# Optimization experiments

Hardware: AMD Instinct MI355X
Metric: run time of the kernel (lower is better)

The kernel has to match this reference:

```python
import jax, jax.numpy as jnp
import numpy as np

B, T, NHANDS, DKP = 8, 1024, 2, 128
DM, H, DH, DFF, V, M, L = 1024, 16, 64, 4096, 2000, 256, 2
KEPS = 1e-4  # performer feature-map epsilon


def _orth_proj(key, m, d):
    # Gaussian orthogonal random features (FAVOR+), rows rescaled to chi norms
    n_blocks = int(np.ceil(m / d))
    blocks = []
    for i in range(n_blocks):
        q, _ = jnp.linalg.qr(jax.random.normal(jax.random.fold_in(key, i), (d, d)))
        blocks.append(q.T)
    mat = jnp.concatenate(blocks, 0)[:m]
    mult = jnp.linalg.norm(jax.random.normal(jax.random.fold_in(key, 10 ** 6), (m, d)), axis=1)
    return (mat * mult[:, None]).astype(jnp.float32)


def setup_inputs() -> dict:
    key = jax.random.key(0)
    ks = iter(jax.random.split(key, 64))
    w = lambda shape, s=0.02: (jax.random.normal(next(ks), shape) * s).astype(jnp.float32)
    z = lambda *shape: jnp.zeros(shape, jnp.float32)
    o = lambda *shape: jnp.ones(shape, jnp.float32)
    return {
        'x': jax.random.normal(next(ks), (B, T, NHANDS, DKP), dtype=jnp.float32),
        'Win': w((NHANDS * DKP, DM)), 'b_in': z(DM),
        'pe': jax.random.normal(next(ks), (5000, DM), dtype=jnp.float32),
        'ln1_g': o(L, DM), 'ln1_b': z(L, DM),
        'Wq': w((L, DM, DM)), 'bq': z(L, DM),
        'Wk': w((L, DM, DM)), 'bk': z(L, DM),
        'Wv': w((L, DM, DM)), 'bv': z(L, DM),
        'Wo': w((L, DM, DM)), 'bo': z(L, DM),
        'ln2_g': o(L, DM), 'ln2_b': z(L, DM),
        'W1': w((L, DM, DFF)), 'b1': z(L, DFF),
        'W2': w((L, DFF, DM)), 'b2': z(L, DM),
        'Wc': w((DM, V)), 'bc': z(V),
        'Wconv': w((64, DM, 3)), 'bconv': z(64),
        'Waux': w((64, V + 1)), 'baux': z(V + 1),
        'proj': _orth_proj(next(ks), M, DH),
    }


def _ln(x, g, b):
    mu = jnp.mean(x, -1, keepdims=True)
    var = jnp.mean((x - mu) ** 2, -1, keepdims=True)
    return (x - mu) / jnp.sqrt(var + 1e-5) * g + b


def _feats(data, proj, is_query):
    # FAVOR+ softmax kernel features, data: (B,H,T,DH) -> (B,H,T,M)
    dn = DH ** -0.25
    ratio = M ** -0.5
    dd = jnp.einsum('bhnd,md->bhnm', data, proj) * dn
    diag = jnp.sum(data ** 2, -1, keepdims=True) * 0.5 * dn * dn
    if is_query:
        stab = jnp.max(dd, -1, keepdims=True)
    else:
        stab = jnp.max(dd, (-1, -2), keepdims=True)
    return ratio * (jnp.exp(dd - diag - jax.lax.stop_gradient(stab)) + KEPS)


def reference(x, Win, b_in, pe, ln1_g, ln1_b, Wq, bq, Wk, bk, Wv, bv, Wo, bo,
              ln2_g, ln2_b, W1, b1, W2, b2, Wc, bc, Wconv, bconv, Waux, baux, proj):
    h = x.reshape(B, T, NHANDS * DKP) @ Win + b_in
    h = h + pe[:T][None]

    def layer(h, i):
        y = _ln(h, ln1_g[i], ln1_b[i])
        q = (y @ Wq[i] + bq[i]).reshape(B, T, H, DH).transpose(0, 2, 1, 3)
        k = (y @ Wk[i] + bk[i]).reshape(B, T, H, DH).transpose(0, 2, 1, 3)
        v = (y @ Wv[i] + bv[i]).reshape(B, T, H, DH).transpose(0, 2, 1, 3)
        qp = _feats(q, proj, True)   # (B,H,T,M)
        kp = _feats(k, proj, False)
        dinv = 1.0 / jnp.einsum('bhnm,bhm->bhn', qp, kp.sum(2))
        ctx = jnp.einsum('bhnm,bhnd->bhmd', kp, v)          # (B,H,M,DH)
        o = jnp.einsum('bhnm,bhmd->bhnd', qp, ctx) * dinv[..., None]
        o = o.transpose(0, 2, 1, 3).reshape(B, T, DM) @ Wo[i] + bo[i]
        h = h + o
        y = _ln(h, ln2_g[i], ln2_b[i])
        ff = jax.nn.gelu(y @ W1[i] + b1[i], approximate=False) @ W2[i] + b2[i]
        return h + ff

    h = layer(h, 0)
    xa = h.transpose(0, 2, 1)  # (B, DM, T)
    xa = jax.lax.conv_general_dilated(xa, Wconv, (1,), 'SAME',
                                      dimension_numbers=('NCH', 'OIH', 'NCH'))
    xa = xa + bconv[None, :, None]
    aux = xa.transpose(0, 2, 1) @ Waux + baux  # (B, T, V+1)
    h = layer(h, 1)
    gloss = h @ Wc + bc  # (B, T, V)
    return (gloss, aux)
```

## Files before the change

### kernel.cpp

```cpp
#include <hip/hip_runtime.h>
#include <hip/hip_bf16.h>

typedef __attribute__((ext_vector_type(4))) float f32x4;
typedef __attribute__((ext_vector_type(8))) unsigned short u16x8;
typedef __attribute__((ext_vector_type(4))) unsigned short u16x4;
typedef __bf16 bf16x8 __attribute__((ext_vector_type(8)));

#define DEVFN static __device__ __forceinline__

constexpr int CB = 8, CT = 1024, CDM = 1024, CH = 16, CDH = 64, CDFF = 4096, CV = 2000, CM = 256;
constexpr int CNT = CB * CT;
constexpr int CQKV = 3072;
constexpr float CDN = 0.35355339059327373f;
constexpr float CRATIO = 0.0625f;
constexpr float CKEPS = 1e-4f;

DEVFN unsigned short f2bu(float x) {
  __hip_bfloat16 h = __float2bfloat16(x);
  return __builtin_bit_cast(unsigned short, h);
}
DEVFN float b2f(unsigned short u) {
  __hip_bfloat16 h = __builtin_bit_cast(__hip_bfloat16, u);
  return __bfloat162float(h);
}
DEVFN float wredsum(float s) {
#pragma unroll
  for (int ofs = 32; ofs; ofs >>= 1) s += __shfl_xor(s, ofs, 64);
  return s;
}
DEVFN float wredmax(float s) {
#pragma unroll
  for (int ofs = 32; ofs; ofs >>= 1) s = fmaxf(s, __shfl_xor(s, ofs, 64));
  return s;
}
DEVFN void gl_lds16(const void* g, void* l) {
  __builtin_amdgcn_global_load_lds(
      (const __attribute__((address_space(1))) unsigned int*)g,
      (__attribute__((address_space(3))) unsigned int*)l, 16, 0, 0);
}
DEVFN f32x4 mfma16(u16x8 a, u16x8 b, f32x4 c) {
  return __builtin_amdgcn_mfma_f32_16x16x32_bf16(
      __builtin_bit_cast(bf16x8, a), __builtin_bit_cast(bf16x8, b), c, 0, 0, 0);
}
DEVFN u16x8 lds_rd128(unsigned addr) {
  u16x8 r;
  asm volatile("ds_read_b128 %0, %1" : "=v"(r) : "v"(addr));
  return r;
}
DEVFN unsigned lds_addr(const void* p) {
  return (unsigned)(unsigned long)(const __attribute__((address_space(3))) char*)p;
}

#define EPI_BIAS 1
#define EPI_ACCUM 2
#define EPI_GELU 4
#define EPI_OUTBF 8
#define EPI_PE 32
#define EPI_DUP 64

template <int EPI>
__global__ __launch_bounds__(512, 4) void gemm128_k(
    const unsigned short* __restrict__ A, const unsigned short* __restrict__ Bt,
    const float* __restrict__ bias, void* __restrict__ C, void* __restrict__ aux,
    int Mr, int Nr, int Kr, int lda, int ldb, int ldc) {
  __shared__ unsigned short smA[2][128 * 64];
  __shared__ unsigned short smB[2][128 * 64];

  int tid = threadIdx.x, wv = tid >> 6, ll = tid & 63;
  int wm = wv >> 2, wn = wv & 3;
  int m0 = blockIdx.x * 128, n0 = blockIdx.y * 128;
  int fr = ll & 15, f16 = ll >> 4, fk = f16 * 8;

  const char* Ab = (const char*)A;
  const char* Bb = (const char*)Bt;

  unsigned int offA[2], offB[2];
#pragma unroll
  for (int ro = 0; ro < 2; ro++) {
    int L = (ro * 512 + tid) * 16;
    int P = L ^ (((L >> 9) & 1) << 5);
    int kh = P >> 13, rem = P & 8191;
    int r = rem >> 6, cb = rem & 63;
    long rowA = min(m0 + r, Mr - 1);
    offA[ro] = (unsigned)((rowA * lda + kh * 32) * 2 + cb);
    long rowB = min(n0 + r, Nr - 1);
    offB[ro] = (unsigned)((rowB * ldb + kh * 32) * 2 + cb);
  }
  unsigned aAb = lds_addr(&smA[0][0]), aBb = lds_addr(&smB[0][0]);
  unsigned offArd[4], offBrd[2];
#pragma unroll
  for (int i = 0; i < 4; i++) {
    int r = wm * 64 + i * 16 + fr;
    offArd[i] = aAb + (unsigned)(r * 64 + 2 * (fk ^ (((r >> 3) & 1) << 4)));
  }
#pragma unroll
  for (int j = 0; j < 2; j++) {
    int r = wn * 32 + j * 16 + fr;
    offBrd[j] = aBb + (unsigned)(r * 64 + 2 * (fk ^ (((r >> 3) & 1) << 4)));
  }

  f32x4 acc[4][2] = {};
  int NT = Kr / 64;

#define STGALL(PB, KBN)                                                      \
  {                                                                          \
    _Pragma("unroll") for (int ro = 0; ro < 2; ro++)                         \
        gl_lds16(Ab + offA[ro] + (KBN), &smA[PB][(ro * 512 + wv * 64) * 8]); \
    _Pragma("unroll") for (int ro = 0; ro < 2; ro++)                         \
        gl_lds16(Bb + offB[ro] + (KBN), &smB[PB][(ro * 512 + wv * 64) * 8]); \
  }
#define TILE(PB, KBN)                                                        \
  {                                                                          \
    __builtin_amdgcn_s_barrier();                                            \
    __builtin_amdgcn_sched_barrier(0);                                       \
    STGALL((PB) ^ 1, KBN);                                                   \
    asm volatile("s_waitcnt vmcnt(4)" ::: "memory");                         \
    __builtin_amdgcn_sched_barrier(0);                                       \
    __builtin_amdgcn_s_barrier();                                            \
    __builtin_amdgcn_sched_barrier(0);                                       \
    u16x8 a0[4], b0[2], a1[4], b1[2];                                        \
    _Pragma("unroll") for (int i = 0; i < 4; i++)                            \
        a0[i] = lds_rd128(offArd[i] + (PB)*16384);                           \
    _Pragma("unroll") for (int j = 0; j < 2; j++)                            \
        b0[j] = lds_rd128(offBrd[j] + (PB)*16384);                           \
    _Pragma("unroll") for (int i = 0; i < 4; i++)                            \
        a1[i] = lds_rd128(offArd[i] + (PB)*16384 + 8192);                    \
    _Pragma("unroll") for (int j = 0; j < 2; j++)                            \
        b1[j] = lds_rd128(offBrd[j] + (PB)*16384 + 8192);                    \
    asm volatile("s_waitcnt lgkmcnt(6)" ::: "memory");                       \
    __builtin_amdgcn_sched_barrier(0);                                       \
    __builtin_amdgcn_s_setprio(1);                                           \
    _Pragma("unroll") for (int i = 0; i < 4; i++) {                          \
      acc[i][0] = mfma16(a0[i], b0[0], acc[i][0]);                           \
      acc[i][1] = mfma16(a0[i], b0[1], acc[i][1]);                           \
    }                                                                        \
    __builtin_amdgcn_s_setprio(0);                                           \
    asm volatile("s_waitcnt lgkmcnt(0)" ::: "memory");                       \
    __builtin_amdgcn_sched_barrier(0);                                       \
    __builtin_amdgcn_s_setprio(1);                                           \
    _Pragma("unroll") for (int i = 0; i < 4; i++) {                          \
      acc[i][0] = mfma16(a1[i], b1[0], acc[i][0]);                           \
      acc[i][1] = mfma16(a1[i], b1[1], acc[i][1]);                           \
    }                                                                        \
    __builtin_amdgcn_s_setprio(0);                                           \
  }

  STGALL(0, 0);
  for (int t = 0; t < NT; t += 2) {
    long kb1 = (long)(t + 1) * 128;
    long kb2 = (long)min(t + 2, NT - 1) * 128;
    TILE(0, kb1);
    TILE(1, kb2);
  }
  asm volatile("s_waitcnt vmcnt(0)" ::: "memory");
  __builtin_amdgcn_sched_barrier(0);
#undef TILE
#undef STGALL

#pragma unroll
  for (int i = 0; i < 4; i++) {
#pragma unroll
    for (int j = 0; j < 2; j++) {
#pragma unroll
      for (int e = 0; e < 4; e++) {
        int gr = m0 + wm * 64 + i * 16 + f16 * 4 + e;
        int gc = n0 + wn * 32 + j * 16 + fr;
        if (gr < Mr && gc < Nr) {
          float v = acc[i][j][e];
          if (EPI & EPI_BIAS) v += bias[gc];
          if (EPI & EPI_GELU) v = 0.5f * v * (1.0f + erff(v * 0.70710678118f));
          if (EPI & EPI_PE) v += ((const float*)aux)[((long)(gr & 1023) << 10) + gc];
          long idx = (long)gr * ldc + gc;
          if (EPI & EPI_ACCUM) v += ((float*)C)[idx];
          if (EPI & EPI_OUTBF) ((unsigned short*)C)[idx] = f2bu(v);
          else ((float*)C)[idx] = v;
          if (EPI & EPI_DUP) ((unsigned short*)aux)[idx] = f2bu(v);
        }
      }
    }
  }
}

template <int EPI, int MB, int NB>
__global__ __launch_bounds__(256) void gemm_k(
    const unsigned short* __restrict__ Aall, const unsigned short* __restrict__ Btall,
    const float* __restrict__ bias, void* __restrict__ Call,
    int Mr, int Nr, int Kr, int lda, int ldb, int ldc, int bdiv,
    long As1, long As2, long Bs1, long Bs2, long Cs1, long Cs2) {
  __shared__ unsigned short smA[MB * 32];
  __shared__ unsigned short smB[NB * 32];
  constexpr int WRN = (MB == 128 && NB == 128) ? 2 : (MB == 128 ? 4 : 1);
  constexpr int WCN = 4 / WRN;
  constexpr int MT = MB / WRN, NTW = NB / WCN;
  constexpr int AF = MT / 16, BF = NTW / 16;
  int bz = blockIdx.z;
  const unsigned short* A = Aall + (long)(bz / bdiv) * As1 + (long)(bz % bdiv) * As2;
  const unsigned short* Bt = Btall + (long)(bz / bdiv) * Bs1 + (long)(bz % bdiv) * Bs2;
  long coff = (long)(bz / bdiv) * Cs1 + (long)(bz % bdiv) * Cs2;

  int tid = threadIdx.x, wv = tid >> 6, ll = tid & 63;
  int m0 = blockIdx.x * MB, n0 = blockIdx.y * NB;
  int sr = tid >> 2, sc = (tid & 3) * 8;
  long ar0 = min(m0 + sr, Mr - 1);
  long ar1 = (MB == 128) ? min(m0 + sr + 64, (long)Mr - 1) : 0;
  long br0 = min(n0 + sr, Nr - 1);
  long br1 = (NB == 128) ? min(n0 + sr + 64, (long)Nr - 1) : 0;
  unsigned short* lA0 = &smA[(wv * 16) * 32];
  unsigned short* lA1 = &smA[(64 + wv * 16) * 32];
  unsigned short* lB0 = &smB[(wv * 16) * 32];
  unsigned short* lB1 = &smB[(64 + wv * 16) * 32];

  f32x4 acc[AF][BF] = {};
  int wr = (WRN == 1) ? 0 : ((WRN == 2) ? (wv >> 1) * MT : wv * MT);
  int wc = (WCN == 1) ? 0 : ((WCN == 2) ? (wv & 1) * NTW : wv * NTW);
  int fr = ll & 15, fk = (ll >> 4) * 8;

  for (int k0 = 0; k0 < Kr; k0 += 32) {
    __syncthreads();
    gl_lds16(A + ar0 * lda + k0 + sc, lA0);
    if (MB == 128) gl_lds16(A + ar1 * lda + k0 + sc, lA1);
    gl_lds16(Bt + br0 * ldb + k0 + sc, lB0);
    if (NB == 128) gl_lds16(Bt + br1 * ldb + k0 + sc, lB1);
    __syncthreads();
    u16x8 af[AF], bfr[BF];
#pragma unroll
    for (int i = 0; i < AF; i++) af[i] = *(const u16x8*)&smA[(wr + i * 16 + fr) * 32 + fk];
#pragma unroll
    for (int j = 0; j < BF; j++) bfr[j] = *(const u16x8*)&smB[(wc + j * 16 + fr) * 32 + fk];
#pragma unroll
    for (int i = 0; i < AF; i++)
#pragma unroll
      for (int j = 0; j < BF; j++) acc[i][j] = mfma16(af[i], bfr[j], acc[i][j]);
  }

#pragma unroll
  for (int i = 0; i < AF; i++) {
#pragma unroll
    for (int j = 0; j < BF; j++) {
#pragma unroll
      for (int e = 0; e < 4; e++) {
        int gr = m0 + wr + i * 16 + (ll >> 4) * 4 + e;
        int gc = n0 + wc + j * 16 + (ll & 15);
        if (gr < Mr && gc < Nr) {
          float v = acc[i][j][e];
          if (EPI & EPI_BIAS) v += bias[gc];
          long idx = coff + (long)gr * ldc + gc;
          if (EPI & EPI_OUTBF) ((unsigned short*)Call)[idx] = f2bu(v);
          else ((float*)Call)[idx] = v;
        }
      }
    }
  }
}

DEVFN void feat_dd(const unsigned short* __restrict__ src, const unsigned short* __restrict__ projc,
                   unsigned short* ldsq, unsigned short* ldsp, int b, int t0, int hh,
                   f32x4 acc[16]) {
  int tid = threadIdx.x, wv = tid >> 6, ll = tid & 63;
#pragma unroll
  for (int p = 0; p < 2; p++) {
    int r = p * 64 + (tid >> 3), c8 = (tid & 7) * 8;
    *(u16x8*)&ldsq[r * 72 + c8] =
        *(const u16x8*)&src[((long)b * CT + t0 + r) * CQKV + hh * CDH + c8];
  }
#pragma unroll
  for (int p = 0; p < 4; p++) {
    int r = p * 64 + (tid >> 3), c8 = (tid & 7) * 8;
    *(u16x8*)&ldsp[r * 72 + c8] = *(const u16x8*)&projc[r * 64 + c8];
  }
  __syncthreads();
  int fr = ll & 15, fk = (ll >> 4) * 8;
#pragma unroll
  for (int ks = 0; ks < 2; ks++) {
    u16x8 af = *(const u16x8*)&ldsq[(wv * 16 + fr) * 72 + ks * 32 + fk];
#pragma unroll
    for (int j = 0; j < 16; j++) {
      u16x8 bf = *(const u16x8*)&ldsp[(j * 16 + fr) * 72 + ks * 32 + fk];
      acc[j] = mfma16(af, bf, acc[j]);
    }
  }
}

__global__ __launch_bounds__(512, 4) void kstab_f(const unsigned short* __restrict__ kb,
                                                  const unsigned short* __restrict__ projc,
                                                  float* __restrict__ part) {
  extern __shared__ char dynsm[];
  unsigned short* ldsq = (unsigned short*)dynsm;
  unsigned short* ldsp = (unsigned short*)(dynsm + 18432);
  __shared__ float smx[8];
  int bh = blockIdx.x >> 3, chunk = blockIdx.x & 7;
  int b = bh >> 4, hh = bh & 15;
  f32x4 acc[16] = {};
  feat_dd(kb, projc, ldsq, ldsp, b, chunk * 128, hh, acc);
  float mx = -3.4e38f;
#pragma unroll
  for (int j = 0; j < 16; j++)
#pragma unroll
    for (int e = 0; e < 4; e++) mx = fmaxf(mx, acc[j][e]);
  mx = wredmax(mx);
  int wv = threadIdx.x >> 6;
  if ((threadIdx.x & 63) == 0) smx[wv] = mx;
  __syncthreads();
  if (threadIdx.x == 0) {
    float m2 = smx[0];
#pragma unroll
    for (int i = 1; i < 8; i++) m2 = fmaxf(m2, smx[i]);
    part[blockIdx.x] = m2;
  }
}

__global__ __launch_bounds__(512, 4) void featk_f(const unsigned short* __restrict__ kb,
                                                  const unsigned short* __restrict__ projc,
                                                  const float* __restrict__ part,
                                                  unsigned short* __restrict__ kpt,
                                                  float* __restrict__ kspart) {
  extern __shared__ char dynsm[];
  unsigned short* ldsq = (unsigned short*)dynsm;
  unsigned short* ldsp = (unsigned short*)(dynsm + 18432);
  unsigned short* ldso = (unsigned short*)dynsm;
  int tid = threadIdx.x, wv = tid >> 6, ll = tid & 63;
  int bh = blockIdx.x >> 3, chunk = blockIdx.x & 7;
  int b = bh >> 4, hh = bh & 15;
  float st = part[bh * 8];
#pragma unroll
  for (int i = 1; i < 8; i++) st = fmaxf(st, part[bh * 8 + i]);
  f32x4 acc[16] = {};
  feat_dd(kb, projc, ldsq, ldsp, b, chunk * 128, hh, acc);
  int fr = ll & 15, g = ll >> 4;
  float diag[4];
#pragma unroll
  for (int e = 0; e < 4; e++) {
    int row = wv * 16 + g * 4 + e;
    u16x4 kv = *(const u16x4*)&ldsq[row * 72 + fr * 4];
    float s = 0;
#pragma unroll
    for (int z = 0; z < 4; z++) { float f = b2f(kv[z]); s += f * f; }
#pragma unroll
    for (int o = 1; o < 16; o <<= 1) s += __shfl_xor(s, o, 64);
    diag[e] = s * (0.5f * CDN * CDN);
  }
  __syncthreads();
#pragma unroll
  for (int j = 0; j < 16; j++)
#pragma unroll
    for (int e = 0; e < 4; e++) {
      float v = CRATIO * (expf(acc[j][e] - diag[e] - st) + CKEPS);
      ldso[(j * 16 + fr) * 136 + wv * 16 + g * 4 + e] = f2bu(v);
    }
  __syncthreads();
  int m = tid >> 1, seg = (tid & 1) * 64;
  long base = ((long)bh * CM + m) * CT + chunk * 128;
  float ks = 0;
#pragma unroll
  for (int z = 0; z < 8; z++) {
    u16x8 v8 = *(u16x8*)&ldso[m * 136 + seg + z * 8];
    *(u16x8*)&kpt[base + seg + z * 8] = v8;
#pragma unroll
    for (int w = 0; w < 8; w++) ks += b2f(v8[w]);
  }
  ks += __shfl_xor(ks, 1, 64);
  if ((tid & 1) == 0) kspart[((long)bh * 8 + chunk) * CM + m] = ks;
}

__global__ __launch_bounds__(512, 4) void featqo_f(const unsigned short* __restrict__ qb,
                                                   const unsigned short* __restrict__ projc,
                                                   const float* __restrict__ kspart,
                                                   const unsigned short* __restrict__ ctxall,
                                                   unsigned short* __restrict__ obuf) {
  extern __shared__ char dynsm[];
  unsigned short* ldsq = (unsigned short*)dynsm;
  unsigned short* ldsp = (unsigned short*)(dynsm + 18432);
  unsigned short* ldso = (unsigned short*)dynsm;
  float* ldks = (float*)(dynsm + 67584);
  float* ldinv = (float*)(dynsm + 68608);
  int tid = threadIdx.x, wv = tid >> 6, ll = tid & 63;
  int bh = blockIdx.x >> 3, chunk = blockIdx.x & 7;
  int b = bh >> 4, hh = bh & 15;
  int t0 = chunk * 128;
  if (tid < 256) {
    float s = 0;
#pragma unroll
    for (int c = 0; c < 8; c++) s += kspart[((long)bh * 8 + c) * CM + tid];
    ldks[tid] = s;
  }
  f32x4 acc[16] = {};
  feat_dd(qb, projc, ldsq, ldsp, b, t0, hh, acc);
  int fr = ll & 15, g = ll >> 4, fk = g * 8;
  float rmax[4], diag[4];
#pragma unroll
  for (int e = 0; e < 4; e++) {
    float mx = acc[0][e];
#pragma unroll
    for (int j = 1; j < 16; j++) mx = fmaxf(mx, acc[j][e]);
#pragma unroll
    for (int o = 1; o < 16; o <<= 1) mx = fmaxf(mx, __shfl_xor(mx, o, 64));
    rmax[e] = mx;
    int row = wv * 16 + g * 4 + e;
    u16x4 qv = *(const u16x4*)&ldsq[row * 72 + fr * 4];
    float s = 0;
#pragma unroll
    for (int z = 0; z < 4; z++) { float f = b2f(qv[z]); s += f * f; }
#pragma unroll
    for (int o = 1; o < 16; o <<= 1) s += __shfl_xor(s, o, 64);
    diag[e] = s * (0.5f * CDN * CDN);
  }
  __syncthreads();
#pragma unroll
  for (int j = 0; j < 16; j++)
#pragma unroll
    for (int e = 0; e < 4; e++) {
      float v = CRATIO * (expf(acc[j][e] - diag[e] - rmax[e]) + CKEPS);
      ldso[(wv * 16 + g * 4 + e) * 264 + j * 16 + fr] = f2bu(v);
    }
  __syncthreads();
  {
    int row = tid >> 2, seg = (tid & 3) * 64;
    float dot = 0;
#pragma unroll
    for (int z = 0; z < 8; z++) {
      u16x8 v8 = *(u16x8*)&ldso[row * 264 + seg + z * 8];
#pragma unroll
      for (int w = 0; w < 8; w++) dot += b2f(v8[w]) * ldks[seg + z * 8 + w];
    }
    dot += __shfl_xor(dot, 1, 64);
    dot += __shfl_xor(dot, 2, 64);
    if ((tid & 3) == 0) ldinv[row] = 1.0f / dot;
  }
  const unsigned short* ctxb = ctxall + (long)bh * 16384;
  f32x4 ao[4] = {};
#pragma unroll
  for (int ks = 0; ks < 8; ks++) {
    u16x8 af = *(const u16x8*)&ldso[(wv * 16 + fr) * 264 + ks * 32 + fk];
#pragma unroll
    for (int j = 0; j < 4; j++) {
      u16x8 bf = *(const u16x8*)&ctxb[(j * 16 + fr) * 256 + ks * 32 + fk];
      ao[j] = mfma16(af, bf, ao[j]);
    }
  }
  __syncthreads();
#pragma unroll
  for (int j = 0; j < 4; j++)
#pragma unroll
    for (int e = 0; e < 4; e++) {
      int r = wv * 16 + g * 4 + e;
      float v = ao[j][e] * ldinv[r];
      obuf[((long)b * CT + t0 + r) * CDM + hh * CDH + j * 16 + fr] = f2bu(v);
    }
}

__global__ __launch_bounds__(256) void ln_k(const float* __restrict__ h,
                                            const float* __restrict__ g,
                                            const float* __restrict__ b,
                                            unsigned short* __restrict__ y) {
  int wv = threadIdx.x >> 6, ll = threadIdx.x & 63;
  long row = (long)blockIdx.x * 4 + wv;
  const float* hr = h + row * CDM;
  f32x4 x[4];
#pragma unroll
  for (int i = 0; i < 4; i++) x[i] = *(const f32x4*)&hr[ll * 16 + i * 4];
  float s = 0;
#pragma unroll
  for (int i = 0; i < 4; i++)
#pragma unroll
    for (int e = 0; e < 4; e++) s += x[i][e];
  float mu = wredsum(s) * (1.f / CDM);
  float v = 0;
#pragma unroll
  for (int i = 0; i < 4; i++)
#pragma unroll
    for (int e = 0; e < 4; e++) {
      float d = x[i][e] - mu;
      v += d * d;
    }
  float inv = rsqrtf(wredsum(v) * (1.f / CDM) + 1e-5f);
  unsigned short o[16];
#pragma unroll
  for (int i = 0; i < 4; i++)
#pragma unroll
    for (int e = 0; e < 4; e++) {
      int c = ll * 16 + i * 4 + e;
      o[i * 4 + e] = f2bu((x[i][e] - mu) * inv * g[c] + b[c]);
    }
  *(u16x8*)&y[row * CDM + ll * 16] = *(u16x8*)&o[0];
  *(u16x8*)&y[row * CDM + ll * 16 + 8] = *(u16x8*)&o[8];
}

__global__ __launch_bounds__(256) void trv_k(const unsigned short* __restrict__ vb,
                                             unsigned short* __restrict__ vt) {
  int bh = blockIdx.x >> 5;
  int t0 = (blockIdx.x & 31) * 32;
  int b = bh >> 4, hh = bh & 15;
  __shared__ unsigned short tile[32][64];
  int tr = threadIdx.x >> 3, dblk = (threadIdx.x & 7) * 8;
  *(u16x8*)&tile[tr][dblk] = *(const u16x8*)&vb[((long)b * CT + t0 + tr) * CQKV + hh * CDH + dblk];
  __syncthreads();
  int d = threadIdx.x >> 2, tz = (threadIdx.x & 3) * 8;
  unsigned short o[8];
#pragma unroll
  for (int e = 0; e < 8; e++) o[e] = tile[tz + e][d];
  *(u16x8*)&vt[((long)bh * CDH + d) * CT + t0 + tz] = *(u16x8*)&o[0];
}

__global__ __launch_bounds__(256) void f2b_k(const float* __restrict__ in,
                                             unsigned short* __restrict__ out, long n) {
  long i = ((long)blockIdx.x * 256 + threadIdx.x) * 4;
  if (i >= n) return;
  f32x4 v = *(const f32x4*)&in[i];
  unsigned short o[4];
#pragma unroll
  for (int e = 0; e < 4; e++) o[e] = f2bu(v[e]);
  *(u16x4*)&out[i] = *(u16x4*)&o[0];
}

__global__ __launch_bounds__(256) void tconvz_k(const float* __restrict__ in,
                                                unsigned short* __restrict__ out, int R, int C,
                                                long szs, long dzs) {
  const float* src = in + (long)blockIdx.z * szs;
  unsigned short* dst = out + (long)blockIdx.z * dzs;
  __shared__ float tile[32][33];
  int r0 = blockIdx.x * 32, c0 = blockIdx.y * 32;
  int tr = threadIdx.x >> 5, tc = threadIdx.x & 31;
#pragma unroll
  for (int p = 0; p < 4; p++) {
    int r = r0 + p * 8 + tr, c = c0 + tc;
    tile[p * 8 + tr][tc] = (r < R && c < C) ? src[(long)r * C + c] : 0.f;
  }
  __syncthreads();
#pragma unroll
  for (int p = 0; p < 4; p++) {
    int c = c0 + p * 8 + tr, r = r0 + tc;
    if (c < C && r < R) dst[(long)c * R + r] = f2bu(tile[tc][p * 8 + tr]);
  }
}

__global__ __launch_bounds__(256) void wconv_k(const float* __restrict__ W,
                                               unsigned short* __restrict__ out) {
  int idx = blockIdx.x * 256 + threadIdx.x;
  int r = idx >> 16, rem = idx & 65535, oc = rem >> 10, ic = rem & 1023;
  out[idx] = f2bu(W[oc * 3072 + ic * 3 + r]);
}

__global__ __launch_bounds__(256) void convmix_k(const float* __restrict__ Y,
                                                 const float* __restrict__ bc,
                                                 unsigned short* __restrict__ xab) {
  long t = (long)blockIdx.x * 4 + (threadIdx.x >> 6);
  int oc = threadIdx.x & 63;
  int tb = (int)(t & 1023);
  float v = Y[t * 192 + 64 + oc] + bc[oc];
  if (tb != 0) v += Y[(t - 1) * 192 + oc];
  if (tb != 1023) v += Y[(t + 1) * 192 + 128 + oc];
  xab[t * 64 + oc] = f2bu(v);
}

__global__ __launch_bounds__(256) void projc_k(const float* __restrict__ p,
                                               unsigned short* __restrict__ out) {
  int i = blockIdx.x * 256 + threadIdx.x;
  out[i] = f2bu(p[i] * CDN);
}

__global__ __launch_bounds__(256) void catb_k(const float* __restrict__ q,
                                              const float* __restrict__ k,
                                              const float* __restrict__ v,
                                              float* __restrict__ o) {
  int l = blockIdx.y;
  int i = blockIdx.x * 256 + threadIdx.x;
  float val = i < 1024 ? q[l * CDM + i] : (i < 2048 ? k[l * CDM + i - 1024] : v[l * CDM + i - 2048]);
  o[l * CQKV + i] = val;
}

#define LAUNCH_GEMM(EPI, MB, NB, A, Bt, bias, C, Mr, Nr, Kr, lda, ldb, ldc, nb, bdiv, As1, As2, Bs1, Bs2, Cs1, Cs2) \
  gemm_k<EPI, MB, NB><<<dim3(((Mr) + (MB)-1) / (MB), ((Nr) + (NB)-1) / (NB), (nb)), 256, 0, stream>>>( \
      (const unsigned short*)(A), (const unsigned short*)(Bt), (bias), (void*)(C),               \
      (Mr), (Nr), (Kr), (lda), (ldb), (ldc), (bdiv), (long)(As1), (long)(As2), (long)(Bs1),      \
      (long)(Bs2), (long)(Cs1), (long)(Cs2))

#define LAUNCH_G1(EPI, A, Bt, bias, C, AUX, Mr, Nr, Kr, lda, ldb, ldc)                           \
  gemm128_k<EPI><<<dim3(((Mr) + 127) / 128, ((Nr) + 127) / 128), 512, 0, stream>>>(              \
      (const unsigned short*)(A), (const unsigned short*)(Bt), (bias), (void*)(C), (void*)(AUX), \
      (Mr), (Nr), (Kr), (lda), (ldb), (ldc))

extern "C" void kernel_launch(void* const* d_in, const int* in_sizes, int n_in,
                              void* d_out, int out_size, void* d_ws, size_t ws_size,
                              hipStream_t stream) {
  const float* x = (const float*)d_in[0];
  const float* Win = (const float*)d_in[1];
  const float* b_in = (const float*)d_in[2];
  const float* pe = (const float*)d_in[3];
  const float* ln1_g = (const float*)d_in[4];
  const float* ln1_b = (const float*)d_in[5];
  const float* Wq = (const float*)d_in[6];
  const float* bq = (const float*)d_in[7];
  const float* Wk = (const float*)d_in[8];
  const float* bk = (const float*)d_in[9];
  const float* Wv = (const float*)d_in[10];
  const float* bv = (const float*)d_in[11];
  const float* Wo = (const float*)d_in[12];
  const float* bo = (const float*)d_in[13];
  const float* ln2_g = (const float*)d_in[14];
  const float* ln2_b = (const float*)d_in[15];
  const float* W1 = (const float*)d_in[16];
  const float* b1 = (const float*)d_in[17];
  const float* W2 = (const float*)d_in[18];
  const float* b2 = (const float*)d_in[19];
  const float* Wc = (const float*)d_in[20];
  const float* bc = (const float*)d_in[21];
  const float* Wconv = (const float*)d_in[22];
  const float* bconv = (const float*)d_in[23];
  const float* Waux = (const float*)d_in[24];
  const float* baux = (const float*)d_in[25];
  const float* proj = (const float*)d_in[26];
  float* out = (float*)d_out;

  char* wsp = (char*)d_ws;
  size_t off = 0;
  auto take = [&](size_t bytes) {
    char* p = wsp + off;
    off = (off + bytes + 255) & ~(size_t)255;
    return p;
  };
  float* h_f = (float*)take(33554432);
  unsigned short* y_bf = (unsigned short*)take(16777216);
  unsigned short* qkv_bf = (unsigned short*)take(50331648);
  unsigned short* kpt_bf = (unsigned short*)take(67108864);
  unsigned short* ff_bf = (unsigned short*)take(67108864);
  unsigned short* ctx_bf = (unsigned short*)take(4194304);
  float* kspart_f = (float*)take(1048576);
  float* kstab_f_buf = (float*)take(4096);
  float* ycv_f = (float*)take(6291456);
  unsigned short* xabf = (unsigned short*)take(1048576);
  float* bqkv_f = (float*)take(24576);
  unsigned short* hbf = (unsigned short*)take(16777216);
  unsigned short* xbf = (unsigned short*)take(4194304);
  unsigned short* win_t = (unsigned short*)take(524288);
  unsigned short* wqkvo_t = (unsigned short*)take(16777216);
  unsigned short* w1_t = (unsigned short*)take(16777216);
  unsigned short* w2_t = (unsigned short*)take(16777216);
  unsigned short* wc_t = (unsigned short*)take(4096000);
  unsigned short* projc = (unsigned short*)take(32768);
  unsigned short* wconv_t = (unsigned short*)take(393216);
  unsigned short* waux_t = (unsigned short*)take(256128);
  unsigned short* vt_bf = y_bf;
  unsigned short* o_bf = y_bf;
  (void)in_sizes; (void)n_in; (void)out_size; (void)ws_size;

  f2b_k<<<2048, 256, 0, stream>>>(x, xbf, (long)CNT * 256);
  tconvz_k<<<dim3(8, 32, 1), 256, 0, stream>>>(Win, win_t, 256, 1024, 0, 0);
  tconvz_k<<<dim3(32, 32, 2), 256, 0, stream>>>(Wq, wqkvo_t + 0 * 1048576, 1024, 1024, 1048576, 4194304);
  tconvz_k<<<dim3(32, 32, 2), 256, 0, stream>>>(Wk, wqkvo_t + 1 * 1048576, 1024, 1024, 1048576, 4194304);
  tconvz_k<<<dim3(32, 32, 2), 256, 0, stream>>>(Wv, wqkvo_t + 2 * 1048576, 1024, 1024, 1048576, 4194304);
  tconvz_k<<<dim3(32, 32, 2), 256, 0, stream>>>(Wo, wqkvo_t + 3 * 1048576, 1024, 1024, 1048576, 4194304);
  tconvz_k<<<dim3(32, 128, 2), 256, 0, stream>>>(W1, w1_t, 1024, 4096, 4194304, 4194304);
  tconvz_k<<<dim3(128, 32, 2), 256, 0, stream>>>(W2, w2_t, 4096, 1024, 4194304, 4194304);
  tconvz_k<<<dim3(32, 63, 1), 256, 0, stream>>>(Wc, wc_t, 1024, 2000, 0, 0);
  tconvz_k<<<dim3(2, 63, 1), 256, 0, stream>>>(Waux, waux_t, 64, 2001, 0, 0);
  catb_k<<<dim3(12, 2), 256, 0, stream>>>(bq, bk, bv, bqkv_f);
  wconv_k<<<768, 256, 0, stream>>>(Wconv, wconv_t);
  projc_k<<<64, 256, 0, stream>>>(proj, projc);

  LAUNCH_G1(EPI_BIAS | EPI_PE, xbf, win_t, b_in, h_f, pe, CNT, CDM, 256, 256, 256, CDM);

  for (int l = 0; l < 2; l++) {
    const unsigned short* wqkv_t = wqkvo_t + (long)(l * 4) * 1048576;
    const unsigned short* wo_t = wqkvo_t + (long)(l * 4 + 3) * 1048576;

    ln_k<<<2048, 256, 0, stream>>>(h_f, ln1_g + l * CDM, ln1_b + l * CDM, y_bf);
    LAUNCH_G1(EPI_BIAS | EPI_OUTBF, y_bf, wqkv_t, bqkv_f + l * CQKV, qkv_bf, nullptr, CNT, CQKV, CDM, CDM, CDM, CQKV);

    kstab_f<<<1024, 512, 55296, stream>>>(qkv_bf + 1024, projc, kstab_f_buf);
    featk_f<<<1024, 512, 69632, stream>>>(qkv_bf + 1024, projc, kstab_f_buf, kpt_bf, kspart_f);
    trv_k<<<4096, 256, 0, stream>>>(qkv_bf + 2048, vt_bf);
    LAUNCH_GEMM(EPI_OUTBF, 64, 128, vt_bf, kpt_bf, nullptr, ctx_bf, CDH, CM, CT, CT, CT, CM, 128, CH,
                (long)CH * CDH * CT, (long)CDH * CT, (long)CH * CM * CT, (long)CM * CT,
                (long)CH * CDH * CM, (long)CDH * CM);
    featqo_f<<<1024, 512, 69120, stream>>>(qkv_bf, projc, kspart_f, ctx_bf, o_bf);
    LAUNCH_G1(EPI_BIAS | EPI_ACCUM, o_bf, wo_t, bo + l * CDM, h_f, nullptr, CNT, CDM, CDM, CDM, CDM, CDM);

    ln_k<<<2048, 256, 0, stream>>>(h_f, ln2_g + l * CDM, ln2_b + l * CDM, y_bf);
    LAUNCH_G1(EPI_BIAS | EPI_GELU | EPI_OUTBF, y_bf, w1_t + (long)l * 4194304, b1 + l * CDFF, ff_bf, nullptr,
              CNT, CDFF, CDM, CDM, CDM, CDFF);
    LAUNCH_G1(EPI_BIAS | EPI_ACCUM | EPI_DUP, ff_bf, w2_t + (long)l * 4194304, b2 + l * CDM, h_f, hbf,
              CNT, CDM, CDFF, CDFF, CDFF, CDM);

    if (l == 0) {
      LAUNCH_GEMM(0, 128, 128, hbf, wconv_t, nullptr, ycv_f, CNT, 192, CDM, CDM, CDM, 192, 1, 1, 0, 0, 0, 0, 0, 0);
      convmix_k<<<2048, 256, 0, stream>>>(ycv_f, bconv, xabf);
      LAUNCH_GEMM(EPI_BIAS, 128, 128, xabf, waux_t, baux, out + 16384000, CNT, CV + 1, 64, 64, 64, CV + 1, 1, 1, 0, 0, 0, 0, 0, 0);
    }
  }

  LAUNCH_G1(EPI_BIAS, hbf, wc_t, bc, out, nullptr, CNT, CV, CDM, CDM, CDM, CV);
}
```

Measured before the change: 1.167 ms.

## Add BK=32 GEMM variant for QKV/FFN1, fuse V transpose into kstab, merge weight converts

New measurement: 1.140 ms (median of 2 runs). -2.3%, faster.

```diff
diff --git a/kernel.cpp b/kernel.cpp
--- a/kernel.cpp
+++ b/kernel.cpp
@@ -57,6 +57,117 @@
 #define EPI_OUTBF 8
 #define EPI_PE 32
 #define EPI_DUP 64
+
+template <int EPI>
+__global__ __launch_bounds__(512, 6) void gemm32_k(
+    const unsigned short* __restrict__ A, const unsigned short* __restrict__ Bt,
+    const float* __restrict__ bias, void* __restrict__ C, void* __restrict__ aux,
+    int Mr, int Nr, int Kr, int lda, int ldb, int ldc) {
+  __shared__ unsigned short smA[2][128 * 32];
+  __shared__ unsigned short smB[2][128 * 32];
+
+  int tid = threadIdx.x, wv = tid >> 6, ll = tid & 63;
+  int wm = wv >> 2, wn = wv & 3;
+  int m0 = blockIdx.x * 128, n0 = blockIdx.y * 128;
+  int fr = ll & 15, f16 = ll >> 4, fk = f16 * 8;
+
+  const char* Ab = (const char*)A;
+  const char* Bb = (const char*)Bt;
+
+  unsigned int offA, offB;
+  {
+    int L = tid * 16;
+    int P = L ^ (((L >> 9) & 1) << 5);
+    int r = P >> 6, cb = P & 63;
+    long rowA = min(m0 + r, Mr - 1);
+    offA = (unsigned)(rowA * lda * 2 + cb);
+    long rowB = min(n0 + r, Nr - 1);
+    offB = (unsigned)(rowB * ldb * 2 + cb);
+  }
+  unsigned aAb = lds_addr(&smA[0][0]), aBb = lds_addr(&smB[0][0]);
+  unsigned offArd[4], offBrd[2];
+#pragma unroll
+  for (int i = 0; i < 4; i++) {
+    int r = wm * 64 + i * 16 + fr;
+    offArd[i] = aAb + (unsigned)(r * 64 + 2 * (fk ^ (((r >> 3) & 1) << 4)));
+  }
+#pragma unroll
+  for (int j = 0; j < 2; j++) {
+    int r = wn * 32 + j * 16 + fr;
+    offBrd[j] = aBb + (unsigned)(r * 64 + 2 * (fk ^ (((r >> 3) & 1) << 4)));
+  }
+
+  f32x4 acc[4][2] = {};
+  int NT = Kr / 32;
+
+#define STG32(PB, KBN)                                                       \
+  {                                                                          \
+    gl_lds16(Ab + offA + (KBN), &smA[PB][tid * 8]);                          \
+    gl_lds16(Bb + offB + (KBN), &smB[PB][tid * 8]);                          \
+  }
+#define TILE32(PB, KBN)                                                      \
+  {                                                                          \
+    __builtin_amdgcn_s_barrier();              \
+    __builtin_amdgcn_sched_barrier(0);                                       \
+    STG32((PB) ^ 1, KBN);                                                    \
+    asm volatile("s_waitcnt vmcnt(2)" ::: "memory");                         \
+    __builtin_amdgcn_sched_barrier(0);                                       \
+    __builtin_amdgcn_s_barrier();                 \
+    __builtin_amdgcn_sched_barrier(0);                                       \
+    u16x8 a[4], b0, b1;                                                      \
+    _Pragma("unroll") for (int i = 0; i < 4; i++)                            \
+        a[i] = lds_rd128(offArd[i] + (PB)*8192);                             \
+    b0 = lds_rd128(offBrd[0] + (PB)*8192);                                   \
+    b1 = lds_rd128(offBrd[1] + (PB)*8192);                                   \
+    asm volatile("s_waitcnt lgkmcnt(1)" ::: "memory");                       \
+    __builtin_amdgcn_sched_barrier(0);                                       \
+    __builtin_amdgcn_s_setprio(1);                                           \
+    _Pragma("unroll") for (int i = 0; i < 4; i++)                            \
+        acc[i][0] = mfma16(a[i], b0, acc[i][0]);                             \
+    __builtin_amdgcn_s_setprio(0);                                           \
+    asm volatile("s_waitcnt lgkmcnt(0)" ::: "memory");                       \
+    __builtin_amdgcn_sched_barrier(0);                                       \
+    __builtin_amdgcn_s_setprio(1);                                           \
+    _Pragma("unroll") for (int i = 0; i < 4; i++)                            \
+        acc[i][1] = mfma16(a[i], b1, acc[i][1]);                             \
+    __builtin_amdgcn_s_setprio(0);                                           \
+  }
+
+  STG32(0, 0);
+  for (int t = 0; t < NT; t += 2) {
+    long kb1 = (long)(t + 1) * 64;
+    long kb2 = (long)min(t + 2, NT - 1) * 64;
+    TILE32(0, kb1);
+    TILE32(1, kb2);
+  }
+  asm volatile("s_waitcnt vmcnt(0)" ::: "memory");
+  __builtin_amdgcn_sched_barrier(0);
+#undef TILE32
+#undef STG32
+
+#pragma unroll
+  for (int i = 0; i < 4; i++) {
+#pragma unroll
+    for (int j = 0; j < 2; j++) {
+#pragma unroll
+      for (int e = 0; e < 4; e++) {
+        int gr = m0 + wm * 64 + i * 16 + f16 * 4 + e;
+        int gc = n0 + wn * 32 + j * 16 + fr;
+        if (gr < Mr && gc < Nr) {
+          float v = acc[i][j][e];
+          if (EPI & EPI_BIAS) v += bias[gc];
+          if (EPI & EPI_GELU) v = 0.5f * v * (1.0f + erff(v * 0.70710678118f));
+          if (EPI & EPI_PE) v += ((const float*)aux)[((long)(gr & 1023) << 10) + gc];
+          long idx = (long)gr * ldc + gc;
+          if (EPI & EPI_ACCUM) v += ((float*)C)[idx];
+          if (EPI & EPI_OUTBF) ((unsigned short*)C)[idx] = f2bu(v);
+          else ((float*)C)[idx] = v;
+          if (EPI & EPI_DUP) ((unsigned short*)aux)[idx] = f2bu(v);
+        }
+      }
+    }
+  }
+}
 
 template <int EPI>
 __global__ __launch_bounds__(512, 4) void gemm128_k(
@@ -283,30 +394,51 @@
 
 __global__ __launch_bounds__(512, 4) void kstab_f(const unsigned short* __restrict__ kb,
                                                   const unsigned short* __restrict__ projc,
-                                                  float* __restrict__ part) {
+                                                  const unsigned short* __restrict__ vb,
+                                                  float* __restrict__ part,
+                                                  unsigned short* __restrict__ vt) {
   extern __shared__ char dynsm[];
   unsigned short* ldsq = (unsigned short*)dynsm;
   unsigned short* ldsp = (unsigned short*)(dynsm + 18432);
   __shared__ float smx[8];
+  int tid = threadIdx.x;
   int bh = blockIdx.x >> 3, chunk = blockIdx.x & 7;
   int b = bh >> 4, hh = bh & 15;
+  int t0 = chunk * 128;
   f32x4 acc[16] = {};
-  feat_dd(kb, projc, ldsq, ldsp, b, chunk * 128, hh, acc);
+  feat_dd(kb, projc, ldsq, ldsp, b, t0, hh, acc);
   float mx = -3.4e38f;
 #pragma unroll
   for (int j = 0; j < 16; j++)
 #pragma unroll
     for (int e = 0; e < 4; e++) mx = fmaxf(mx, acc[j][e]);
   mx = wredmax(mx);
-  int wv = threadIdx.x >> 6;
-  if ((threadIdx.x & 63) == 0) smx[wv] = mx;
-  __syncthreads();
-  if (threadIdx.x == 0) {
+  int wv = tid >> 6;
+  if ((tid & 63) == 0) smx[wv] = mx;
+  __syncthreads();
+  if (tid == 0) {
     float m2 = smx[0];
 #pragma unroll
     for (int i = 1; i < 8; i++) m2 = fmaxf(m2, smx[i]);
     part[blockIdx.x] = m2;
   }
+#pragma unroll
+  for (int p = 0; p < 2; p++) {
+    int r = p * 64 + (tid >> 3), c8 = (tid & 7) * 8;
+    *(u16x8*)&ldsq[r * 72 + c8] =
+        *(const u16x8*)&vb[((long)b * CT + t0 + r) * CQKV + hh * CDH + c8];
+  }
+  __syncthreads();
+  int d = tid >> 3, tz = (tid & 7) * 16;
+  unsigned short o1[8], o2[8];
+#pragma unroll
+  for (int e = 0; e < 8; e++) {
+    o1[e] = ldsq[(tz + e) * 72 + d];
+    o2[e] = ldsq[(tz + 8 + e) * 72 + d];
+  }
+  long vbase = ((long)bh * CDH + d) * CT + t0 + tz;
+  *(u16x8*)&vt[vbase] = *(u16x8*)&o1[0];
+  *(u16x8*)&vt[vbase + 8] = *(u16x8*)&o2[0];
 }
 
 __global__ __launch_bounds__(512, 4) void featk_f(const unsigned short* __restrict__ kb,
@@ -485,22 +617,6 @@
   *(u16x8*)&y[row * CDM + ll * 16 + 8] = *(u16x8*)&o[8];
 }
 
-__global__ __launch_bounds__(256) void trv_k(const unsigned short* __restrict__ vb,
-                                             unsigned short* __restrict__ vt) {
-  int bh = blockIdx.x >> 5;
-  int t0 = (blockIdx.x & 31) * 32;
-  int b = bh >> 4, hh = bh & 15;
-  __shared__ unsigned short tile[32][64];
-  int tr = threadIdx.x >> 3, dblk = (threadIdx.x & 7) * 8;
-  *(u16x8*)&tile[tr][dblk] = *(const u16x8*)&vb[((long)b * CT + t0 + tr) * CQKV + hh * CDH + dblk];
-  __syncthreads();
-  int d = threadIdx.x >> 2, tz = (threadIdx.x & 3) * 8;
-  unsigned short o[8];
-#pragma unroll
-  for (int e = 0; e < 8; e++) o[e] = tile[tz + e][d];
-  *(u16x8*)&vt[((long)bh * CDH + d) * CT + t0 + tz] = *(u16x8*)&o[0];
-}
-
 __global__ __launch_bounds__(256) void f2b_k(const float* __restrict__ in,
                                              unsigned short* __restrict__ out, long n) {
   long i = ((long)blockIdx.x * 256 + threadIdx.x) * 4;
@@ -530,6 +646,30 @@
   for (int p = 0; p < 4; p++) {
     int c = c0 + p * 8 + tr, r = r0 + tc;
     if (c < C && r < R) dst[(long)c * R + r] = f2bu(tile[tc][p * 8 + tr]);
+  }
+}
+
+__global__ __launch_bounds__(256) void tconv4_k(const float* __restrict__ Wq,
+                                                const float* __restrict__ Wk,
+                                                const float* __restrict__ Wv,
+                                                const float* __restrict__ Wo,
+                                                unsigned short* __restrict__ out) {
+  int w = blockIdx.z & 3, l = blockIdx.z >> 2;
+  const float* src = (w == 0 ? Wq : w == 1 ? Wk : w == 2 ? Wv : Wo) + (long)l * 1048576;
+  unsigned short* dst = out + ((long)l * 4 + w) * 1048576;
+  __shared__ float tile[32][33];
+  int r0 = blockIdx.x * 32, c0 = blockIdx.y * 32;
+  int tr = threadIdx.x >> 5, tc = threadIdx.x & 31;
+#pragma unroll
+  for (int p = 0; p < 4; p++) {
+    int r = r0 + p * 8 + tr, c = c0 + tc;
+    tile[p * 8 + tr][tc] = src[(long)r * 1024 + c];
+  }
+  __syncthreads();
+#pragma unroll
+  for (int p = 0; p < 4; p++) {
+    int c = c0 + p * 8 + tr, r = r0 + tc;
+    dst[(long)c * 1024 + r] = f2bu(tile[tc][p * 8 + tr]);
   }
 }
 
@@ -576,6 +716,11 @@
 
 #define LAUNCH_G1(EPI, A, Bt, bias, C, AUX, Mr, Nr, Kr, lda, ldb, ldc)                           \
   gemm128_k<EPI><<<dim3(((Mr) + 127) / 128, ((Nr) + 127) / 128), 512, 0, stream>>>(              \
+      (const unsigned short*)(A), (const unsigned short*)(Bt), (bias), (void*)(C), (void*)(AUX), \
+      (Mr), (Nr), (Kr), (lda), (ldb), (ldc))
+
+#define LAUNCH_G32(EPI, A, Bt, bias, C, AUX, Mr, Nr, Kr, lda, ldb, ldc)                          \
+  gemm32_k<EPI><<<dim3(((Mr) + 127) / 128, ((Nr) + 127) / 128), 512, 0, stream>>>(               \
       (const unsigned short*)(A), (const unsigned short*)(Bt), (bias), (void*)(C), (void*)(AUX), \
       (Mr), (Nr), (Kr), (lda), (ldb), (ldc))
 
@@ -645,10 +790,7 @@
 
   f2b_k<<<2048, 256, 0, stream>>>(x, xbf, (long)CNT * 256);
   tconvz_k<<<dim3(8, 32, 1), 256, 0, stream>>>(Win, win_t, 256, 1024, 0, 0);
-  tconvz_k<<<dim3(32, 32, 2), 256, 0, stream>>>(Wq, wqkvo_t + 0 * 1048576, 1024, 1024, 1048576, 4194304);
-  tconvz_k<<<dim3(32, 32, 2), 256, 0, stream>>>(Wk, wqkvo_t + 1 * 1048576, 1024, 1024, 1048576, 4194304);
-  tconvz_k<<<dim3(32, 32, 2), 256, 0, stream>>>(Wv, wqkvo_t + 2 * 1048576, 1024, 1024, 1048576, 4194304);
-  tconvz_k<<<dim3(32, 32, 2), 256, 0, stream>>>(Wo, wqkvo_t + 3 * 1048576, 1024, 1024, 1048576, 4194304);
+  tconv4_k<<<dim3(32, 32, 8), 256, 0, stream>>>(Wq, Wk, Wv, Wo, wqkvo_t);
   tconvz_k<<<dim3(32, 128, 2), 256, 0, stream>>>(W1, w1_t, 1024, 4096, 4194304, 4194304);
   tconvz_k<<<dim3(128, 32, 2), 256, 0, stream>>>(W2, w2_t, 4096, 1024, 4194304, 4194304);
   tconvz_k<<<dim3(32, 63, 1), 256, 0, stream>>>(Wc, wc_t, 1024, 2000, 0, 0);
@@ -664,11 +806,10 @@
     const unsigned short* wo_t = wqkvo_t + (long)(l * 4 + 3) * 1048576;
 
     ln_k<<<2048, 256, 0, stream>>>(h_f, ln1_g + l * CDM, ln1_b + l * CDM, y_bf);
-    LAUNCH_G1(EPI_BIAS | EPI_OUTBF, y_bf, wqkv_t, bqkv_f + l * CQKV, qkv_bf, nullptr, CNT, CQKV, CDM, CDM, CDM, CQKV);
-
-    kstab_f<<<1024, 512, 55296, stream>>>(qkv_bf + 1024, projc, kstab_f_buf);
+    LAUNCH_G32(EPI_BIAS | EPI_OUTBF, y_bf, wqkv_t, bqkv_f + l * CQKV, qkv_bf, nullptr, CNT, CQKV, CDM, CDM, CDM, CQKV);
+
+    kstab_f<<<1024, 512, 55296, stream>>>(qkv_bf + 1024, projc, qkv_bf + 2048, kstab_f_buf, vt_bf);
     featk_f<<<1024, 512, 69632, stream>>>(qkv_bf + 1024, projc, kstab_f_buf, kpt_bf, kspart_f);
-    trv_k<<<4096, 256, 0, stream>>>(qkv_bf + 2048, vt_bf);
     LAUNCH_GEMM(EPI_OUTBF, 64, 128, vt_bf, kpt_bf, nullptr, ctx_bf, CDH, CM, CT, CT, CT, CM, 128, CH,
                 (long)CH * CDH * CT, (long)CDH * CT, (long)CH * CM * CT, (long)CM * CT,
                 (long)CH * CDH * CM, (long)CDH * CM);
@@ -676,8 +817,8 @@
     LAUNCH_G1(EPI_BIAS | EPI_ACCUM, o_bf, wo_t, bo + l * CDM, h_f, nullptr, CNT, CDM, CDM, CDM, CDM, CDM);
 
     ln_k<<<2048, 256, 0, stream>>>(h_f, ln2_g + l * CDM, ln2_b + l * CDM, y_bf);
-    LAUNCH_G1(EPI_BIAS | EPI_GELU | EPI_OUTBF, y_bf, w1_t + (long)l * 4194304, b1 + l * CDFF, ff_bf, nullptr,
-              CNT, CDFF, CDM, CDM, CDM, CDFF);
+    LAUNCH_G32(EPI_BIAS | EPI_GELU | EPI_OUTBF, y_bf, w1_t + (long)l * 4194304, b1 + l * CDFF, ff_bf, nullptr,
+               CNT, CDFF, CDM, CDM, CDM, CDFF);
     LAUNCH_G1(EPI_BIAS | EPI_ACCUM | EPI_DUP, ff_bf, w2_t + (long)l * 4194304, b2 + l * CDM, h_f, hbf,
               CNT, CDM, CDFF, CDFF, CDFF, CDM);
 
```
